# Kernel optimization log

Measured on AMD Instinct MI355X. Metric: run time of the kernel, lower is better.

## Reference

```python
import jax, jax.numpy as jnp
import numpy as np

B, S, HID = 16, 512, 2048
H = 4
D = HID // H  # 512; module requires S == D
SCALE = 1.0 / np.sqrt(D).astype(np.float32)


def setup_inputs() -> dict:
    key = jax.random.key(0)
    ks = jax.random.split(key, 6)
    std = 0.02
    inp = {"hidden_states": jax.random.normal(ks[0], (B, S, HID), jnp.float32)}
    names = ["q", "k", "v", "ck", "cv"]
    for i, n in enumerate(names):
        inp[f"W{n}"] = jax.random.normal(ks[i + 1], (HID, HID), jnp.float32) * std
        inp[f"b{n}"] = jnp.zeros((HID,), jnp.float32)
    return inp


def _heads(x):
    # [B,S,HID] -> [B,H,S,D]
    return x.reshape(B, S, H, D).transpose(0, 2, 1, 3)


def reference(hidden_states, Wq, bq, Wk, bk, Wv, bv, Wck, bck, Wcv, bcv):
    q = _heads(hidden_states @ Wq.T + bq)
    k = _heads(hidden_states @ Wk.T + bk)
    v = _heads(hidden_states @ Wv.T + bv)
    ck = _heads(hidden_states @ Wck.T + bck)
    cv = _heads(hidden_states @ Wcv.T + bcv)

    # scores1[b,h,q,j] = sum_d Q[b,h,q,d] K[b,h,j,d]
    s1 = jnp.einsum('bhqd,bhjd->bhqj', q, k)
    # scores2 = scores1 @ cube_key^T (valid since S == D)
    s2 = jnp.einsum('bhqj,bhmj->bhqm', s1, ck) * SCALE
    probs = jax.nn.softmax(s2, axis=-1)
    # ctx1 = probs @ V : [B,H,S,D]
    ctx = jnp.einsum('bhqm,bhmd->bhqd', probs, v)
    # ctx2 = ctx1 @ cube_value : [S,D]@[S,D] valid since S == D
    ctx = jnp.einsum('bhqm,bhme->bhqe', ctx, cv)
    # merge heads: [B,H,S,D] -> [B,S,HID]
    return ctx.transpose(0, 2, 1, 3).reshape(B, S, HID)
```

## Files before the change

### kernel.cpp

```cpp
#include <hip/hip_runtime.h>
#include <math.h>


typedef _Float16 f16;
typedef f16 f16x8 __attribute__((ext_vector_type(8)));
typedef float f32x4 __attribute__((ext_vector_type(4)));
typedef float f32x16 __attribute__((ext_vector_type(16)));

#define SB_STRIDE 520
#define BP_HALF   16384
#define CHAIN_LDS ((64 * SB_STRIDE + 2 * BP_HALF) * 2)
#define PROJ_LDS  131072

static constexpr float SCALE = 0.04419417382415922f;

__device__ __forceinline__ void gl_lds16(const f16* g, f16* l)
{
    __builtin_amdgcn_global_load_lds(
        (const __attribute__((address_space(1))) void*)g,
        (__attribute__((address_space(3))) void*)l, 16, 0, 0);
}

__global__ __launch_bounds__(256) void conv_f32_f16(const float* __restrict__ src,
                                                    f16* __restrict__ dst, int n)
{
    int i = (blockIdx.x * 256 + threadIdx.x) * 8;
    if (i + 8 <= n) {
        float4 a = *(const float4*)(src + i);
        float4 b = *(const float4*)(src + i + 4);
        f16 o[8] = {(f16)a.x, (f16)a.y, (f16)a.z, (f16)a.w,
                    (f16)b.x, (f16)b.y, (f16)b.z, (f16)b.w};
        *(int4*)(dst + i) = *(int4*)o;
    }
}

struct ProjPtrs {
    const f16* W[5];
    const float* bias[5];
    f16* dst[5];
};

__global__ __launch_bounds__(512, 2) void proj_f16(const f16* __restrict__ A, ProjPtrs P)
{
    extern __shared__ f16 sm[];
    const int z = blockIdx.z;
    const f16* __restrict__ W = P.W[z];
    const float* __restrict__ bias = P.bias[z];
    f16* __restrict__ dst = P.dst[z];
    const bool tr = (z == 2) || (z == 4);

    const int t    = threadIdx.x;
    const int lane = t & 63;
    const int wave = t >> 6;
    const int wr   = wave >> 2, wc = wave & 3;
    const int bm = blockIdx.y * 256, bn = blockIdx.x * 256;
    const int r16 = lane & 15;
    const int kq  = lane >> 4;

    const f16* gA = A + (size_t)(bm + (wave >> 1) * 16 + r16) * 2048 + ((wave & 1) * 4 + kq) * 8;
    const f16* gB = W + (size_t)(bn + (wave >> 1) * 16 + r16) * 2048 + ((wave & 1) * 4 + kq) * 8;
    const int stoff = wave * 512;

#define STG_A(c, h, tt)                                                     \
    {                                                                       \
        f16* d_ = sm + (c) * 32768 + (h) * 8192 + stoff;                    \
        gl_lds16(gA + (size_t)((h) * 128) * 2048 + (tt) * 64, d_);          \
        gl_lds16(gA + (size_t)((h) * 128 + 64) * 2048 + (tt) * 64, d_ + 4096); \
    }
#define STG_B(c, h, tt)                                                     \
    {                                                                       \
        f16* d_ = sm + (c) * 32768 + 16384 + (h) * 8192 + stoff;            \
        gl_lds16(gB + (size_t)((h) * 128) * 2048 + (tt) * 64, d_);          \
        gl_lds16(gB + (size_t)((h) * 128 + 64) * 2048 + (tt) * 64, d_ + 4096); \
    }

    f32x4 acc[8][4];
#pragma unroll
    for (int mf = 0; mf < 8; ++mf)
#pragma unroll
        for (int nf = 0; nf < 4; ++nf)
#pragma unroll
            for (int r = 0; r < 4; ++r) acc[mf][nf][r] = 0.f;

    STG_A(0, 0, 0); STG_A(0, 1, 0); STG_B(0, 0, 0); STG_B(0, 1, 0);
    STG_A(1, 0, 1); STG_A(1, 1, 1);
    asm volatile("s_waitcnt vmcnt(4)" ::: "memory");
    __builtin_amdgcn_s_barrier();
    asm volatile("" ::: "memory");

    const int aoff = kq * 128 + r16 * 8;

    f16x8 af[8][2], bf[4][2];

    for (int kt = 0; kt < 32; ++kt) {
        const int cur = kt & 1, nxt = cur ^ 1;
        const f16* pa = sm + cur * 32768 + wr * 8192 + aoff;
        const f16* pb = sm + cur * 32768 + 16384 + (wc >> 1) * 8192 + (wc & 1) * 4096 + aoff;

#pragma unroll
        for (int mf = 0; mf < 4; ++mf)
#pragma unroll
            for (int dk = 0; dk < 2; ++dk)
                af[mf][dk] = *(const f16x8*)(pa + mf * 1024 + dk * 512);
#pragma unroll
        for (int nf = 0; nf < 2; ++nf)
#pragma unroll
            for (int dk = 0; dk < 2; ++dk)
                bf[nf][dk] = *(const f16x8*)(pb + nf * 1024 + dk * 512);
        if (kt + 1 < 32) STG_B(nxt, 0, kt + 1);
        asm volatile("" ::: "memory");
        __builtin_amdgcn_s_barrier();
        asm volatile("s_waitcnt lgkmcnt(0)" ::: "memory");
        __builtin_amdgcn_sched_barrier(0);
        __builtin_amdgcn_s_setprio(1);
#pragma unroll
        for (int mf = 0; mf < 4; ++mf)
#pragma unroll
            for (int nf = 0; nf < 2; ++nf)
#pragma unroll
                for (int dk = 0; dk < 2; ++dk)
                    acc[mf][nf] = __builtin_amdgcn_mfma_f32_16x16x32_f16(
                        af[mf][dk], bf[nf][dk], acc[mf][nf], 0, 0, 0);
        __builtin_amdgcn_s_setprio(0);
        asm volatile("" ::: "memory");
        __builtin_amdgcn_s_barrier();
        asm volatile("" ::: "memory");

#pragma unroll
        for (int mf = 4; mf < 8; ++mf)
#pragma unroll
            for (int dk = 0; dk < 2; ++dk)
                af[mf][dk] = *(const f16x8*)(pa + mf * 1024 + dk * 512);
        if (kt + 1 < 32) STG_B(nxt, 1, kt + 1);
        asm volatile("" ::: "memory");
        __builtin_amdgcn_s_barrier();
        asm volatile("s_waitcnt lgkmcnt(0)" ::: "memory");
        __builtin_amdgcn_sched_barrier(0);
        __builtin_amdgcn_s_setprio(1);
#pragma unroll
        for (int mf = 4; mf < 8; ++mf)
#pragma unroll
            for (int nf = 0; nf < 2; ++nf)
#pragma unroll
                for (int dk = 0; dk < 2; ++dk)
                    acc[mf][nf] = __builtin_amdgcn_mfma_f32_16x16x32_f16(
                        af[mf][dk], bf[nf][dk], acc[mf][nf], 0, 0, 0);
        __builtin_amdgcn_s_setprio(0);
        asm volatile("" ::: "memory");
        __builtin_amdgcn_s_barrier();
        asm volatile("" ::: "memory");

#pragma unroll
        for (int nf = 2; nf < 4; ++nf)
#pragma unroll
            for (int dk = 0; dk < 2; ++dk)
                bf[nf][dk] = *(const f16x8*)(pb + nf * 1024 + dk * 512);
        if (kt + 2 < 32) STG_A(cur, 0, kt + 2);
        asm volatile("" ::: "memory");
        __builtin_amdgcn_s_barrier();
        asm volatile("s_waitcnt lgkmcnt(0)" ::: "memory");
        __builtin_amdgcn_sched_barrier(0);
        __builtin_amdgcn_s_setprio(1);
#pragma unroll
        for (int mf = 0; mf < 4; ++mf)
#pragma unroll
            for (int nf = 2; nf < 4; ++nf)
#pragma unroll
                for (int dk = 0; dk < 2; ++dk)
                    acc[mf][nf] = __builtin_amdgcn_mfma_f32_16x16x32_f16(
                        af[mf][dk], bf[nf][dk], acc[mf][nf], 0, 0, 0);
        __builtin_amdgcn_s_setprio(0);
        asm volatile("" ::: "memory");
        __builtin_amdgcn_s_barrier();
        asm volatile("" ::: "memory");

        if (kt + 2 < 32) STG_A(cur, 1, kt + 2);
        if (kt < 30) asm volatile("s_waitcnt vmcnt(4)" ::: "memory");
        else         asm volatile("s_waitcnt vmcnt(0)" ::: "memory");
        __builtin_amdgcn_s_barrier();
        asm volatile("" ::: "memory");
        __builtin_amdgcn_s_setprio(1);
#pragma unroll
        for (int mf = 4; mf < 8; ++mf)
#pragma unroll
            for (int nf = 2; nf < 4; ++nf)
#pragma unroll
                for (int dk = 0; dk < 2; ++dk)
                    acc[mf][nf] = __builtin_amdgcn_mfma_f32_16x16x32_f16(
                        af[mf][dk], bf[nf][dk], acc[mf][nf], 0, 0, 0);
        __builtin_amdgcn_s_setprio(0);
        asm volatile("" ::: "memory");
        __builtin_amdgcn_s_barrier();
        asm volatile("" ::: "memory");
    }
#undef STG_A
#undef STG_B

    const int wm = wr * 128, wn = wc * 64;
#pragma unroll
    for (int nf = 0; nf < 4; ++nf) {
        int n = bn + wn + nf * 16 + r16;
        float bb = bias[n];
        int h = n >> 9, d = n & 511;
#pragma unroll
        for (int mf = 0; mf < 8; ++mf) {
            int mbase = bm + wm + mf * 16 + (lane >> 4) * 4;
            int b = mbase >> 9, s0 = mbase & 511;
            if (!tr) {
#pragma unroll
                for (int r = 0; r < 4; ++r)
                    dst[(((size_t)(b * 4 + h)) * 512 + s0 + r) * 512 + d] =
                        (f16)(acc[mf][nf][r] + bb);
            } else {
                f16 pk[4];
#pragma unroll
                for (int r = 0; r < 4; ++r) pk[r] = (f16)(acc[mf][nf][r] + bb);
                *(float2*)(dst + (((size_t)(b * 4 + h)) * 512 + d) * 512 + s0) =
                    *(float2*)pk;
            }
        }
    }
}

__device__ __forceinline__ void stage_nt(
    const f16* __restrict__ Bsrc,
    f16* __restrict__ Sb, f16* __restrict__ Bp, int t, f32x16 acc[2][2])
{
    const int lane = t & 63;
    const int wave = t >> 6;
    const int l31  = lane & 31;
    const int l5   = (lane >> 5) * 8;

#pragma unroll
    for (int mt = 0; mt < 2; ++mt)
#pragma unroll
        for (int nt = 0; nt < 2; ++nt)
#pragma unroll
            for (int r = 0; r < 16; ++r) acc[mt][nt][r] = 0.f;

#pragma unroll
    for (int it = 0; it < 4; ++it) {
        int nb = wave * 2 + (it & 1), ks = it >> 1;
        gl_lds16(Bsrc + (size_t)(nb * 32 + l31) * 512 + ks * 16 + l5,
                 Bp + nb * 1024 + ks * 512);
    }

    for (int p = 0; p < 16; ++p) {
        const int k0 = p * 32;
        __syncthreads();
        if (p < 15) {
            f16* nbuf = Bp + ((p + 1) & 1) * BP_HALF;
#pragma unroll
            for (int it = 0; it < 4; ++it) {
                int nb = wave * 2 + (it & 1), ks = it >> 1;
                gl_lds16(Bsrc + (size_t)(nb * 32 + l31) * 512 + k0 + 32 + ks * 16 + l5,
                         nbuf + nb * 1024 + ks * 512);
            }
        }
        const f16* cbuf = Bp + (p & 1) * BP_HALF;
#pragma unroll
        for (int dk = 0; dk < 32; dk += 16) {
            f16x8 af[2], bf[2];
#pragma unroll
            for (int mt = 0; mt < 2; ++mt)
                af[mt] = *(const f16x8*)(Sb + (size_t)(mt * 32 + l31) * SB_STRIDE + k0 + dk + l5);
#pragma unroll
            for (int nt = 0; nt < 2; ++nt)
                bf[nt] = *(const f16x8*)(cbuf + (wave * 2 + nt) * 1024 + (dk >> 4) * 512 + lane * 8);
#pragma unroll
            for (int mt = 0; mt < 2; ++mt)
#pragma unroll
                for (int nt = 0; nt < 2; ++nt)
                    acc[mt][nt] = __builtin_amdgcn_mfma_f32_32x32x16_f16(af[mt], bf[nt], acc[mt][nt], 0, 0, 0);
        }
    }
    __syncthreads();
}

__device__ __forceinline__ void emit_to_S(f16* __restrict__ Sb, const f32x16 acc[2][2],
                                          int t, float scale)
{
    const int lane = t & 63;
    const int wn = (t >> 6) * 64;
#pragma unroll
    for (int mt = 0; mt < 2; ++mt)
#pragma unroll
        for (int nt = 0; nt < 2; ++nt) {
            int col = wn + nt * 32 + (lane & 31);
#pragma unroll
            for (int r = 0; r < 16; ++r) {
                int row = mt * 32 + (r & 3) + 8 * (r >> 2) + 4 * (lane >> 5);
                Sb[(size_t)row * SB_STRIDE + col] = (f16)(acc[mt][nt][r] * scale);
            }
        }
}

__global__ __launch_bounds__(512) void chain_f16(
    const f16* __restrict__ q16, const f16* __restrict__ k16,
    const f16* __restrict__ ck16, const f16* __restrict__ vt16,
    const f16* __restrict__ cvt16, float* __restrict__ out)
{
    extern __shared__ f16 smem[];
    f16* Sb = smem;
    f16* Bp = smem + 64 * SB_STRIDE;
    const int t = threadIdx.x;
    const int bh = blockIdx.x >> 3;
    const int q0 = (blockIdx.x & 7) * 64;
    const size_t SB = 512 * 512;

    const f16* Q = q16 + bh * SB;
    for (int i = t; i < 4096; i += 512) {
        int row = i >> 6, c = (i & 63) * 8;
        *(int4*)(Sb + (size_t)row * SB_STRIDE + c) =
            *(const int4*)(Q + (size_t)(q0 + row) * 512 + c);
    }

    f32x16 acc[2][2];

    stage_nt(k16 + bh * SB, Sb, Bp, t, acc);
    emit_to_S(Sb, acc, t, 1.0f);

    stage_nt(ck16 + bh * SB, Sb, Bp, t, acc);
    emit_to_S(Sb, acc, t, SCALE);
    __syncthreads();

    {
        const int lane = t & 63;
        const int wave = t >> 6;
        for (int rr = 0; rr < 8; ++rr) {
            int r = wave * 8 + rr;
            f16x8 xv = *(const f16x8*)(Sb + (size_t)r * SB_STRIDE + lane * 8);
            float x[8];
            float mx = -1e30f;
#pragma unroll
            for (int j = 0; j < 8; ++j) { x[j] = (float)xv[j]; mx = fmaxf(mx, x[j]); }
#pragma unroll
            for (int o = 32; o > 0; o >>= 1) mx = fmaxf(mx, __shfl_xor(mx, o));
            float s = 0.f;
#pragma unroll
            for (int j = 0; j < 8; ++j) { x[j] = __expf(x[j] - mx); s += x[j]; }
#pragma unroll
            for (int o = 32; o > 0; o >>= 1) s += __shfl_xor(s, o);
            float inv = 1.0f / s;
            f16x8 ov;
#pragma unroll
            for (int j = 0; j < 8; ++j) ov[j] = (f16)(x[j] * inv);
            *(f16x8*)(Sb + (size_t)r * SB_STRIDE + lane * 8) = ov;
        }
    }

    stage_nt(vt16 + bh * SB, Sb, Bp, t, acc);
    emit_to_S(Sb, acc, t, 1.0f);

    stage_nt(cvt16 + bh * SB, Sb, Bp, t, acc);
    {
        const int lane = t & 63;
        const int wn = (t >> 6) * 64;
        int b = bh >> 2, h = bh & 3;
#pragma unroll
        for (int mt = 0; mt < 2; ++mt)
#pragma unroll
            for (int nt = 0; nt < 2; ++nt) {
                int col = h * 512 + wn + nt * 32 + (lane & 31);
#pragma unroll
                for (int r = 0; r < 16; ++r) {
                    int row = q0 + mt * 32 + (r & 3) + 8 * (r >> 2) + 4 * (lane >> 5);
                    out[((size_t)b * 512 + row) * 2048 + col] = acc[mt][nt][r];
                }
            }
    }
}

extern "C" void kernel_launch(void* const* d_in, const int* in_sizes, int n_in,
                              void* d_out, int out_size, void* d_ws, size_t ws_size,
                              hipStream_t stream)
{
    const float* hs = (const float*)d_in[0];
    const float* Wf[5] = {(const float*)d_in[1], (const float*)d_in[3],
                          (const float*)d_in[5], (const float*)d_in[7],
                          (const float*)d_in[9]};
    const float* bf[5] = {(const float*)d_in[2], (const float*)d_in[4],
                          (const float*)d_in[6], (const float*)d_in[8],
                          (const float*)d_in[10]};
    float* out = (float*)d_out;

    hipFuncSetAttribute((const void*)chain_f16,
                        hipFuncAttributeMaxDynamicSharedMemorySize, CHAIN_LDS);
    hipFuncSetAttribute((const void*)proj_f16,
                        hipFuncAttributeMaxDynamicSharedMemorySize, PROJ_LDS);

    f16* ws = (f16*)d_ws;
    const size_t WELEM = 2048ULL * 2048;
    const size_t FULLACT = 64ULL * 512 * 512;

    f16* W16[5];
    for (int i = 0; i < 5; ++i) W16[i] = ws + i * WELEM;
    f16* after_w = ws + 5 * WELEM;

    for (int i = 0; i < 5; ++i)
        conv_f32_f16<<<dim3(WELEM / 2048), 256, 0, stream>>>(Wf[i], W16[i], (int)WELEM);

    size_t full_need = (5 * WELEM + FULLACT + 5 * FULLACT) * sizeof(f16);
    if (ws_size >= full_need) {
        f16* hs16 = after_w;
        f16* act[5];
        for (int i = 0; i < 5; ++i) act[i] = after_w + FULLACT + i * FULLACT;

        conv_f32_f16<<<dim3(FULLACT / 2048), 256, 0, stream>>>(hs, hs16, (int)FULLACT);

        ProjPtrs P;
        for (int i = 0; i < 5; ++i) { P.W[i] = W16[i]; P.bias[i] = bf[i]; P.dst[i] = act[i]; }
        proj_f16<<<dim3(8, 32, 5), 512, PROJ_LDS, stream>>>(hs16, P);

        chain_f16<<<dim3(512), 512, CHAIN_LDS, stream>>>(
            act[0], act[1], act[3], act[2], act[4], out);
    } else {
        const size_t CHROW = 1048576ULL;
        const size_t CHACT = 4ULL * 512 * 512;
        f16* hs16c = after_w;
        f16* act[5];
        for (int i = 0; i < 5; ++i) act[i] = after_w + CHROW + i * CHACT;

        ProjPtrs P;
        for (int i = 0; i < 5; ++i) { P.W[i] = W16[i]; P.bias[i] = bf[i]; P.dst[i] = act[i]; }

        for (int c = 0; c < 16; ++c) {
            conv_f32_f16<<<dim3(CHROW / 2048), 256, 0, stream>>>(
                hs + c * CHROW, hs16c, (int)CHROW);
            proj_f16<<<dim3(8, 2, 5), 512, PROJ_LDS, stream>>>(hs16c, P);
            chain_f16<<<dim3(32), 512, CHAIN_LDS, stream>>>(
                act[0], act[1], act[3], act[2], act[4], out + c * CHROW);
        }
    }

    (void)in_sizes; (void)n_in; (void)out_size;
}
```

Baseline: 765.0 us.

## Load B operand fragments straight into registers instead of staging through LDS

Each wave only ever uses its own 64 columns of the B matrix, so the chain stages now load those fragments from global memory directly into registers with a two-deep register prefetch, instead of staging them through a double-buffered LDS tile with a barrier every k-step. This removes the per-iteration __syncthreads and shrinks LDS use to the 64-row score tile. Launch bounds now request 4 blocks per CU so more blocks can be resident and hide global latency. The cost is more VGPR pressure, direct global loads whose per-lane layout may be less coalesced, and the risk that the compiler spills under the tighter occupancy bound.

```diff
diff --git a/kernel.cpp b/kernel.cpp
--- a/kernel.cpp
+++ b/kernel.cpp
@@ -8,8 +8,7 @@
 typedef float f32x16 __attribute__((ext_vector_type(16)));
 
 #define SB_STRIDE 520
-#define BP_HALF   16384
-#define CHAIN_LDS ((64 * SB_STRIDE + 2 * BP_HALF) * 2)
+#define CHAIN_LDS (64 * SB_STRIDE * 2)
 #define PROJ_LDS  131072
 
 static constexpr float SCALE = 0.04419417382415922f;
@@ -222,9 +221,9 @@
     }
 }
 
-__device__ __forceinline__ void stage_nt(
-    const f16* __restrict__ Bsrc,
-    f16* __restrict__ Sb, f16* __restrict__ Bp, int t, f32x16 acc[2][2])
+__device__ __forceinline__ void stage_ntr(const f16* __restrict__ Bsrc,
+                                          const f16* __restrict__ Sb,
+                                          int t, f32x16 acc[2][2])
 {
     const int lane = t & 63;
     const int wave = t >> 6;
@@ -238,43 +237,37 @@
 #pragma unroll
             for (int r = 0; r < 16; ++r) acc[mt][nt][r] = 0.f;
 
-#pragma unroll
-    for (int it = 0; it < 4; ++it) {
-        int nb = wave * 2 + (it & 1), ks = it >> 1;
-        gl_lds16(Bsrc + (size_t)(nb * 32 + l31) * 512 + ks * 16 + l5,
-                 Bp + nb * 1024 + ks * 512);
-    }
-
+    const f16* b0 = Bsrc + (size_t)(wave * 64 + l31) * 512 + l5;
+    const f16* b1 = Bsrc + (size_t)(wave * 64 + 32 + l31) * 512 + l5;
+
+    f16x8 bfA[2][2], bfB[2][2];
+
+#define LDP(S, pp)                                              \
+    do {                                                        \
+        S[0][0] = *(const f16x8*)(b0 + (pp) * 32);              \
+        S[0][1] = *(const f16x8*)(b0 + (pp) * 32 + 16);         \
+        S[1][0] = *(const f16x8*)(b1 + (pp) * 32);              \
+        S[1][1] = *(const f16x8*)(b1 + (pp) * 32 + 16);         \
+    } while (0)
+
+    LDP(bfA, 0);
+    LDP(bfB, 1);
+
+#pragma unroll
     for (int p = 0; p < 16; ++p) {
-        const int k0 = p * 32;
-        __syncthreads();
-        if (p < 15) {
-            f16* nbuf = Bp + ((p + 1) & 1) * BP_HALF;
-#pragma unroll
-            for (int it = 0; it < 4; ++it) {
-                int nb = wave * 2 + (it & 1), ks = it >> 1;
-                gl_lds16(Bsrc + (size_t)(nb * 32 + l31) * 512 + k0 + 32 + ks * 16 + l5,
-                         nbuf + nb * 1024 + ks * 512);
-            }
+        f16x8 (&S)[2][2] = (p & 1) ? bfB : bfA;
+#pragma unroll
+        for (int dkh = 0; dkh < 2; ++dkh) {
+            f16x8 af0 = *(const f16x8*)(Sb + (size_t)l31 * SB_STRIDE + p * 32 + dkh * 16 + l5);
+            f16x8 af1 = *(const f16x8*)(Sb + (size_t)(32 + l31) * SB_STRIDE + p * 32 + dkh * 16 + l5);
+            acc[0][0] = __builtin_amdgcn_mfma_f32_32x32x16_f16(af0, S[0][dkh], acc[0][0], 0, 0, 0);
+            acc[0][1] = __builtin_amdgcn_mfma_f32_32x32x16_f16(af0, S[1][dkh], acc[0][1], 0, 0, 0);
+            acc[1][0] = __builtin_amdgcn_mfma_f32_32x32x16_f16(af1, S[0][dkh], acc[1][0], 0, 0, 0);
+            acc[1][1] = __builtin_amdgcn_mfma_f32_32x32x16_f16(af1, S[1][dkh], acc[1][1], 0, 0, 0);
         }
-        const f16* cbuf = Bp + (p & 1) * BP_HALF;
-#pragma unroll
-        for (int dk = 0; dk < 32; dk += 16) {
-            f16x8 af[2], bf[2];
-#pragma unroll
-            for (int mt = 0; mt < 2; ++mt)
-                af[mt] = *(const f16x8*)(Sb + (size_t)(mt * 32 + l31) * SB_STRIDE + k0 + dk + l5);
-#pragma unroll
-            for (int nt = 0; nt < 2; ++nt)
-                bf[nt] = *(const f16x8*)(cbuf + (wave * 2 + nt) * 1024 + (dk >> 4) * 512 + lane * 8);
-#pragma unroll
-            for (int mt = 0; mt < 2; ++mt)
-#pragma unroll
-                for (int nt = 0; nt < 2; ++nt)
-                    acc[mt][nt] = __builtin_amdgcn_mfma_f32_32x32x16_f16(af[mt], bf[nt], acc[mt][nt], 0, 0, 0);
-        }
-    }
-    __syncthreads();
+        if (p + 2 < 16) LDP(S, p + 2);
+    }
+#undef LDP
 }
 
 __device__ __forceinline__ void emit_to_S(f16* __restrict__ Sb, const f32x16 acc[2][2],
@@ -295,14 +288,13 @@
         }
 }
 
-__global__ __launch_bounds__(512) void chain_f16(
+__global__ __launch_bounds__(512, 4) void chain_f16(
     const f16* __restrict__ q16, const f16* __restrict__ k16,
     const f16* __restrict__ ck16, const f16* __restrict__ vt16,
     const f16* __restrict__ cvt16, float* __restrict__ out)
 {
     extern __shared__ f16 smem[];
     f16* Sb = smem;
-    f16* Bp = smem + 64 * SB_STRIDE;
     const int t = threadIdx.x;
     const int bh = blockIdx.x >> 3;
     const int q0 = (blockIdx.x & 7) * 64;
@@ -314,13 +306,17 @@
         *(int4*)(Sb + (size_t)row * SB_STRIDE + c) =
             *(const int4*)(Q + (size_t)(q0 + row) * 512 + c);
     }
+    __syncthreads();
 
     f32x16 acc[2][2];
 
-    stage_nt(k16 + bh * SB, Sb, Bp, t, acc);
+    stage_ntr(k16 + bh * SB, Sb, t, acc);
+    __syncthreads();
     emit_to_S(Sb, acc, t, 1.0f);
-
-    stage_nt(ck16 + bh * SB, Sb, Bp, t, acc);
+    __syncthreads();
+
+    stage_ntr(ck16 + bh * SB, Sb, t, acc);
+    __syncthreads();
     emit_to_S(Sb, acc, t, SCALE);
     __syncthreads();
 
@@ -348,11 +344,14 @@
             *(f16x8*)(Sb + (size_t)r * SB_STRIDE + lane * 8) = ov;
         }
     }
-
-    stage_nt(vt16 + bh * SB, Sb, Bp, t, acc);
+    __syncthreads();
+
+    stage_ntr(vt16 + bh * SB, Sb, t, acc);
+    __syncthreads();
     emit_to_S(Sb, acc, t, 1.0f);
-
-    stage_nt(cvt16 + bh * SB, Sb, Bp, t, acc);
+    __syncthreads();
+
+    stage_ntr(cvt16 + bh * SB, Sb, t, acc);
     {
         const int lane = t & 63;
         const int wn = (t >> 6) * 64;
```

New measurement: 769.5 us. No clear change (+0.6%).
